# Kernel tuning notes

Measured on AMD Instinct MI355X. Metric: run time of the kernel, lower is better.

The kernel has to match this reference:

```python
import jax, jax.numpy as jnp
import numpy as np

EPS = 1e-6
PRED_LEN = 336
K_DETACH = 6

def expmap0(v):
    # tangent v [..., E] at Lorentz origin (k=1) -> point [..., E+1]
    r = jnp.linalg.norm(v, axis=-1, keepdims=True)
    x0 = jnp.cosh(r)
    scale = jnp.where(r > EPS, jnp.sinh(r) / jnp.maximum(r, EPS), 1.0)
    return jnp.concatenate([x0, scale * v], axis=-1)

def logmap0(x):
    # Lorentz point [..., E+1] -> tangent [..., E] at origin (k=1)
    x0 = jnp.clip(x[..., :1], 1.0, None)
    xs = x[..., 1:]
    r = jnp.arccosh(x0)
    n = jnp.linalg.norm(xs, axis=-1, keepdims=True)
    return r * xs / jnp.maximum(n, EPS)

def setup_inputs():
    key = jax.random.key(0)
    ks = jax.random.split(key, 16)
    B, T, C = 128, 2048, 128
    E, H, L = 32, 64, 2048
    w = lambda k, s: jax.random.normal(k, s, jnp.float32) * 0.02
    z = lambda s: jnp.zeros(s, jnp.float32)
    return dict(
        x=jax.random.normal(ks[0], (B, T, C), jnp.float32),
        We_trend=w(ks[1], (L, E)), be_trend=z((E,)),
        We_weekly=w(ks[2], (L, E)), be_weekly=z((E,)),
        We_daily=w(ks[3], (L, E)), be_daily=z((E,)),
        We_resid=w(ks[4], (L, E)), be_resid=z((E,)),
        Wd_in=w(ks[5], (E, H)), bd_in=z((H,)),
        Wd_gate=w(ks[6], (E, H)), bd_gate=z((H,)),
        Wd_out=w(ks[7], (H, E)), bd_out=z((E,)),
        Wr=w(ks[8], (E, C)), br=z((C,)),
    )

def _forward(x, We_trend, be_trend, We_weekly, be_weekly, We_daily, be_daily,
             We_resid, be_resid, Wd_in, bd_in, Wd_gate, bd_gate, Wd_out, bd_out, Wr, br):
    B, T, C = x.shape
    k = min(7, T // 4)
    if k > 1:
        xp = jnp.pad(x, ((0, 0), (k // 2, k // 2), (0, 0)), mode='edge')  # replicate pad on time
        cs = jnp.cumsum(xp, axis=1)
        cs = jnp.concatenate([jnp.zeros((B, 1, C), x.dtype), cs], axis=1)
        trend = (cs[:, k:, :] - cs[:, :-k, :]) / k  # avg_pool1d(kernel=k, stride=1) -> [B,T,C]
    else:
        trend = x
    residual = x - trend
    # only channel 0 is consumed downstream
    t0 = trend[:, :, 0]       # [B, T]
    r0 = residual[:, :, 0]    # weekly == daily == resid == residual[:, :, 0]
    # ParallelLorentzBlock: per-component lookback projection, tanh, sum, lift to Lorentz
    v = (jnp.tanh(t0 @ We_trend + be_trend)
         + jnp.tanh(r0 @ We_weekly + be_weekly)
         + jnp.tanh(r0 @ We_daily + be_daily)
         + jnp.tanh(r0 @ We_resid + be_resid))  # [B, E]
    z0 = expmap0(v)  # combined_h on Lorentz manifold [B, E+1]
    masks = ((jnp.arange(PRED_LEN) + 1) % K_DETACH) == 0

    def step(z, m):
        tv = logmap0(z)  # [B, E]
        u = jax.nn.silu(tv @ Wd_in + bd_in) * jax.nn.sigmoid(tv @ Wd_gate + bd_gate)  # gated Mamba-style update
        vn = tv + u @ Wd_out + bd_out
        zn = expmap0(vn)
        x_pred = logmap0(zn) @ Wr + br  # reconstruction head -> [B, C]
        zc = jnp.where(m, jax.lax.stop_gradient(zn), zn)  # periodic detach every K steps
        return zc, x_pred

    _, preds = jax.lax.scan(step, z0, masks)  # [pred_len, B, C]
    return jnp.transpose(preds, (1, 0, 2))    # [B, pred_len, C]

def reference(x, We_trend, be_trend, We_weekly, be_weekly, We_daily, be_daily,
              We_resid, be_resid, Wd_in, bd_in, Wd_gate, bd_gate, Wd_out, bd_out, Wr, br):
    return _forward(x, We_trend, be_trend, We_weekly, be_weekly, We_daily, be_daily,
                    We_resid, be_resid, Wd_in, bd_in, Wd_gate, bd_gate, Wd_out, bd_out, Wr, br)
```

## Files before the change

kernel.cpp:

```cpp
#include <hip/hip_runtime.h>

typedef float v2f __attribute__((ext_vector_type(2)));

#define T_LEN 2048
#define BB    128
#define CC    128
#define EE    32
#define HH    64
#define PRED  336
#define CH    28
#define NCH   12

#define WS_MAG 0
#define WS_MR  8192
#define WS_CAG 16384
#define WS_CR  16512
#define WS_V   16640

__device__ __forceinline__ v2f mk2(float a, float b) { v2f t; t.x = a; t.y = b; return t; }

__device__ __forceinline__ float swap_sum1(float X, float Y) {
    unsigned x = __builtin_bit_cast(unsigned, X);
    unsigned y = __builtin_bit_cast(unsigned, Y);
#if __has_builtin(__builtin_amdgcn_permlane32_swap)
    auto r = __builtin_amdgcn_permlane32_swap(x, y, false, false);
    return __builtin_bit_cast(float, (unsigned)r[0]) +
           __builtin_bit_cast(float, (unsigned)r[1]);
#else
    asm("v_permlane32_swap_b32 %0, %1" : "+v"(x), "+v"(y));
    return __builtin_bit_cast(float, x) + __builtin_bit_cast(float, y);
#endif
}

__device__ __forceinline__ v2f swap_sum(v2f X, v2f Y) {
    v2f z;
    z.x = swap_sum1(X.x, Y.x);
    z.y = swap_sum1(X.y, Y.y);
    return z;
}

#define ROWS(F) F(0) F(1) F(2) F(3) F(4) F(5) F(6) F(7) F(8) F(9) F(10) F(11) \
                F(12) F(13) F(14) F(15) F(16) F(17) F(18) F(19) F(20) F(21)   \
                F(22) F(23) F(24) F(25) F(26) F(27) F(28) F(29) F(30) F(31)
#define DECLM(r) v2f mA##r, mB##r;
#define INITM(r) mA##r = Mrow[(rbase + r) * HH + p];      \
                 mB##r = Mrow[(rbase + r) * HH + p + 32];
#define FMAQ(q, a, b, c, d)                               \
    X0 += q.x * mA##a;  Y0 += q.x * mB##a;                \
    X1 += q.y * mA##b;  Y1 += q.y * mB##b;                \
    X0 += q.z * mA##c;  Y0 += q.z * mB##c;                \
    X1 += q.w * mA##d;  Y1 += q.w * mB##d;
#define FMA_ALL                                           \
    FMAQ(q0,  0,  1,  2,  3)  FMAQ(q1,  4,  5,  6,  7)    \
    FMAQ(q2,  8,  9, 10, 11)  FMAQ(q3, 12, 13, 14, 15)    \
    FMAQ(q4, 16, 17, 18, 19)  FMAQ(q5, 20, 21, 22, 23)    \
    FMAQ(q6, 24, 25, 26, 27)  FMAQ(q7, 28, 29, 30, 31)

__global__ __launch_bounds__(256) void prep_kernel(
    const float* __restrict__ x,
    const float* __restrict__ WeT, const float* __restrict__ beT,
    const float* __restrict__ WeW, const float* __restrict__ beW,
    const float* __restrict__ WeD, const float* __restrict__ beD,
    const float* __restrict__ WeR, const float* __restrict__ beR,
    const float* __restrict__ Wdin, const float* __restrict__ Wdg,
    const float* __restrict__ Wdo,  const float* __restrict__ bdo,
    const float* __restrict__ Wr,
    float* __restrict__ ws)
{
    const int tid = threadIdx.x;

    if (blockIdx.x < BB) {
        __shared__ __align__(16) float s_x [T_LEN + 6];
        __shared__ __align__(16) float s_tr[T_LEN];
        __shared__ __align__(16) float s_rs[T_LEN];
        __shared__ __align__(16) float s_part[4][8][32];

        const int b = blockIdx.x;
        const float* xb = x + (size_t)b * T_LEN * CC;

        for (int i = tid; i < T_LEN + 6; i += 256) {
            int t = i - 3;
            t = t < 0 ? 0 : (t > T_LEN - 1 ? T_LEN - 1 : t);
            s_x[i] = xb[(size_t)t * CC];
        }
        __syncthreads();

        for (int t = tid; t < T_LEN; t += 256) {
            float s = 0.f;
            #pragma unroll
            for (int j = 0; j < 7; ++j) s += s_x[t + j];
            float tm = s * (1.0f / 7.0f);
            s_tr[t] = tm;
            s_rs[t] = s_x[t + 3] - tm;
        }
        __syncthreads();

        {
            const int e = tid & 31, tg = tid >> 5;
            float a0 = 0.f, a1 = 0.f, a2 = 0.f, a3 = 0.f;
            #pragma unroll 4
            for (int j = 0; j < 256; ++j) {
                int lt = tg * 256 + j;
                int wi = lt * EE + e;
                float trv = s_tr[lt], rsv = s_rs[lt];
                a0 += trv * WeT[wi];
                a1 += rsv * WeW[wi];
                a2 += rsv * WeD[wi];
                a3 += rsv * WeR[wi];
            }
            s_part[0][tg][e] = a0;
            s_part[1][tg][e] = a1;
            s_part[2][tg][e] = a2;
            s_part[3][tg][e] = a3;
        }
        __syncthreads();

        if (tid < EE) {
            float s0 = 0.f, s1 = 0.f, s2 = 0.f, s3 = 0.f;
            #pragma unroll
            for (int g = 0; g < 8; ++g) {
                s0 += s_part[0][g][tid];
                s1 += s_part[1][g][tid];
                s2 += s_part[2][g][tid];
                s3 += s_part[3][g][tid];
            }
            ws[WS_V + b * EE + tid] =
                  tanhf(s0 + beT[tid]) + tanhf(s1 + beW[tid])
                + tanhf(s2 + beD[tid]) + tanhf(s3 + beR[tid]);
        }
        return;
    }

    const int t0 = (blockIdx.x - BB) * 256 + tid;
    const int hp = t0 >> 6;
    const int j  = t0 & 63;
    float mi = 0.f, mg = 0.f, r0 = 0.f, r1 = 0.f;
    #pragma unroll 4
    for (int e = 0; e < EE; ++e) {
        float wo = Wdo[hp * EE + e];
        mi += wo * Wdin[e * HH + j];
        mg += wo * Wdg [e * HH + j];
        r0 += wo * Wr  [e * CC + 2 * j];
        r1 += wo * Wr  [e * CC + 2 * j + 1];
    }
    ws[WS_MAG + (hp * HH + j) * 2    ] = mi;
    ws[WS_MAG + (hp * HH + j) * 2 + 1] = mg;
    ws[WS_MR  + hp * CC + 2 * j      ] = r0;
    ws[WS_MR  + hp * CC + 2 * j + 1  ] = r1;

    if (t0 < HH) {
        float ci = 0.f, cg = 0.f;
        for (int e = 0; e < EE; ++e) {
            float bo = bdo[e];
            ci += bo * Wdin[e * HH + t0];
            cg += bo * Wdg [e * HH + t0];
        }
        ws[WS_CAG + t0 * 2    ] = ci;
        ws[WS_CAG + t0 * 2 + 1] = cg;
    } else if (t0 < HH + CC) {
        int c = t0 - HH;
        float cr = 0.f;
        for (int e = 0; e < EE; ++e) cr += bdo[e] * Wr[e * CC + c];
        ws[WS_CR + c] = cr;
    }
}

__global__ __launch_bounds__(128, 1) void scan_kernel(
    const float* __restrict__ ws,
    const float* __restrict__ Wdin, const float* __restrict__ bdin,
    const float* __restrict__ Wdg,  const float* __restrict__ bdg,
    const float* __restrict__ Wr,   const float* __restrict__ br,
    float* __restrict__ out)
{
    __shared__ __align__(16) float s_v[EE];
    __shared__ __align__(16) float s_u[2][CH][HH];

    const int tid  = threadIdx.x;
    const int wid  = tid >> 6;
    const int lane = tid & 63;
    const int half = lane >> 5;
    const int p    = lane & 31;
    const int b    = blockIdx.x;

    if (tid < EE) s_v[tid] = ws[WS_V + b * EE + tid];
    __syncthreads();

    if (wid == 0) {
        const v2f* Mrow = (const v2f*)(ws + WS_MAG);
        const int rbase = half << 5;
        ROWS(DECLM)
        ROWS(INITM)
        const v2f c_ag = ((const v2f*)(ws + WS_CAG))[lane];

        v2f ag = mk2(bdin[lane], bdg[lane]);
        {
            v2f t0 = mk2(0.f, 0.f), t1 = mk2(0.f, 0.f);
            for (int e = 0; e < EE; e += 2) {
                float v0 = s_v[e], v1 = s_v[e + 1];
                t0.x += v0 * Wdin[e * HH + lane];
                t0.y += v0 * Wdg [e * HH + lane];
                t1.x += v1 * Wdin[(e + 1) * HH + lane];
                t1.y += v1 * Wdg [(e + 1) * HH + lane];
            }
            ag += t0 + t1;
        }

        for (int c = 0; c < NCH + 1; ++c) {
            if (c < NCH) {
                float* ring = &s_u[c & 1][0][0];
                for (int i = 0; i < CH; ++i) {
                    float a = ag.x, g = ag.y;
                    float ea = __expf(-a), eg = __expf(-g);
                    float u = a * __builtin_amdgcn_rcpf((1.f + ea) * (1.f + eg));
                    ring[i * HH + lane] = u;

                    const float4* u4 = (const float4*)(ring + i * HH + (half << 5));
                    float4 q0 = u4[0], q1 = u4[1], q2 = u4[2], q3 = u4[3];
                    float4 q4 = u4[4], q5 = u4[5], q6 = u4[6], q7 = u4[7];
                    v2f X0 = mk2(0.f, 0.f), X1 = mk2(0.f, 0.f);
                    v2f Y0 = mk2(0.f, 0.f), Y1 = mk2(0.f, 0.f);
                    FMA_ALL
                    ag += swap_sum(X0 + X1, Y0 + Y1) + c_ag;
                }
            }
            __syncthreads();
        }
    } else {
        const v2f* Mrow = (const v2f*)(ws + WS_MR);
        const int rbase = half << 5;
        ROWS(DECLM)
        ROWS(INITM)
        const v2f c_r2 = ((const v2f*)(ws + WS_CR))[lane];

        v2f P = ((const v2f*)br)[lane];
        {
            v2f t0 = mk2(0.f, 0.f), t1 = mk2(0.f, 0.f);
            for (int e = 0; e < EE; e += 2) {
                t0 += s_v[e]     * ((const v2f*)(Wr + e * CC))[lane];
                t1 += s_v[e + 1] * ((const v2f*)(Wr + (e + 1) * CC))[lane];
            }
            P += t0 + t1;
        }

        v2f* outb = (v2f*)(out + (size_t)b * PRED * CC);

        for (int c = 0; c < NCH + 1; ++c) {
            if (c > 0) {
                const float* ring = &s_u[(c - 1) & 1][0][0];
                const int n0 = (c - 1) * CH;
                for (int i = 0; i < CH; ++i) {
                    const float4* u4 = (const float4*)(ring + i * HH + (half << 5));
                    float4 q0 = u4[0], q1 = u4[1], q2 = u4[2], q3 = u4[3];
                    float4 q4 = u4[4], q5 = u4[5], q6 = u4[6], q7 = u4[7];
                    v2f X0 = mk2(0.f, 0.f), X1 = mk2(0.f, 0.f);
                    v2f Y0 = mk2(0.f, 0.f), Y1 = mk2(0.f, 0.f);
                    FMA_ALL
                    P += swap_sum(X0 + X1, Y0 + Y1) + c_r2;
                    outb[(size_t)(n0 + i) * (CC / 2) + lane] = P;
                }
            }
            __syncthreads();
        }
    }
}

extern "C" void kernel_launch(void* const* d_in, const int* in_sizes, int n_in,
                              void* d_out, int out_size, void* d_ws, size_t ws_size,
                              hipStream_t stream)
{
    const float* x    = (const float*)d_in[0];
    const float* WeT  = (const float*)d_in[1];
    const float* beT  = (const float*)d_in[2];
    const float* WeW  = (const float*)d_in[3];
    const float* beW  = (const float*)d_in[4];
    const float* WeD  = (const float*)d_in[5];
    const float* beD  = (const float*)d_in[6];
    const float* WeR  = (const float*)d_in[7];
    const float* beR  = (const float*)d_in[8];
    const float* Wdin = (const float*)d_in[9];
    const float* bdin = (const float*)d_in[10];
    const float* Wdg  = (const float*)d_in[11];
    const float* bdg  = (const float*)d_in[12];
    const float* Wdo  = (const float*)d_in[13];
    const float* bdo  = (const float*)d_in[14];
    const float* Wr   = (const float*)d_in[15];
    const float* br   = (const float*)d_in[16];

    float* ws  = (float*)d_ws;
    float* out = (float*)d_out;

    prep_kernel<<<BB + 16, 256, 0, stream>>>(x, WeT, beT, WeW, beW, WeD, beD,
                                             WeR, beR, Wdin, Wdg, Wdo, bdo,
                                             Wr, ws);
    scan_kernel<<<BB, 128, 0, stream>>>(ws, Wdin, bdin, Wdg, bdg, Wr, br, out);
}
```

Measured before the change: 345.4 us.

## Broadcast gate activations via readlane and stream transposed weight matrix from memory

Result: slower. 353.8 us (+2.5%).

```diff
diff --git a/kernel.cpp b/kernel.cpp
--- a/kernel.cpp
+++ b/kernel.cpp
@@ -18,6 +18,14 @@
 #define WS_V   16640
 
 __device__ __forceinline__ v2f mk2(float a, float b) { v2f t; t.x = a; t.y = b; return t; }
+
+__device__ __forceinline__ float bcast(unsigned ub, int k) {
+#if __has_builtin(__builtin_amdgcn_readlane)
+    return __builtin_bit_cast(float, (unsigned)__builtin_amdgcn_readlane((int)ub, k));
+#else
+    return __builtin_bit_cast(float, (unsigned)__shfl((int)ub, k, 64));
+#endif
+}
 
 __device__ __forceinline__ float swap_sum1(float X, float Y) {
     unsigned x = __builtin_bit_cast(unsigned, X);
@@ -56,6 +64,16 @@
     FMAQ(q4, 16, 17, 18, 19)  FMAQ(q5, 20, 21, 22, 23)    \
     FMAQ(q6, 24, 25, 26, 27)  FMAQ(q7, 28, 29, 30, 31)
 
+#define PGRP(g, ACC)                                                        \
+    _Pragma("unroll")                                                       \
+    for (int k2 = 0; k2 < 8; ++k2) {                                        \
+        float4 mm = Mcol4[(g) * 8 + k2];                                    \
+        float s0 = bcast(ub, (g) * 16 + 2 * k2);                            \
+        float s1 = bcast(ub, (g) * 16 + 2 * k2 + 1);                        \
+        ACC.x += s0 * mm.x;  ACC.y += s0 * mm.y;                            \
+        ACC.x += s1 * mm.z;  ACC.y += s1 * mm.w;                            \
+    }
+
 __global__ __launch_bounds__(256) void prep_kernel(
     const float* __restrict__ x,
     const float* __restrict__ WeT, const float* __restrict__ beT,
@@ -143,8 +161,8 @@
         r0 += wo * Wr  [e * CC + 2 * j];
         r1 += wo * Wr  [e * CC + 2 * j + 1];
     }
-    ws[WS_MAG + (hp * HH + j) * 2    ] = mi;
-    ws[WS_MAG + (hp * HH + j) * 2 + 1] = mg;
+    ws[WS_MAG + (j * HH + hp) * 2    ] = mi;
+    ws[WS_MAG + (j * HH + hp) * 2 + 1] = mg;
     ws[WS_MR  + hp * CC + 2 * j      ] = r0;
     ws[WS_MR  + hp * CC + 2 * j + 1  ] = r1;
 
@@ -186,10 +204,7 @@
     __syncthreads();
 
     if (wid == 0) {
-        const v2f* Mrow = (const v2f*)(ws + WS_MAG);
-        const int rbase = half << 5;
-        ROWS(DECLM)
-        ROWS(INITM)
+        const float4* Mcol4 = (const float4*)(ws + WS_MAG) + lane * (HH / 2);
         const v2f c_ag = ((const v2f*)(ws + WS_CAG))[lane];
 
         v2f ag = mk2(bdin[lane], bdg[lane]);
@@ -214,13 +229,16 @@
                     float u = a * __builtin_amdgcn_rcpf((1.f + ea) * (1.f + eg));
                     ring[i * HH + lane] = u;
 
-                    const float4* u4 = (const float4*)(ring + i * HH + (half << 5));
-                    float4 q0 = u4[0], q1 = u4[1], q2 = u4[2], q3 = u4[3];
-                    float4 q4 = u4[4], q5 = u4[5], q6 = u4[6], q7 = u4[7];
-                    v2f X0 = mk2(0.f, 0.f), X1 = mk2(0.f, 0.f);
-                    v2f Y0 = mk2(0.f, 0.f), Y1 = mk2(0.f, 0.f);
-                    FMA_ALL
-                    ag += swap_sum(X0 + X1, Y0 + Y1) + c_ag;
+                    const unsigned ub = __builtin_bit_cast(unsigned, u);
+                    v2f A0 = c_ag;
+                    v2f A1 = mk2(0.f, 0.f);
+                    v2f A2 = mk2(0.f, 0.f);
+                    v2f A3 = mk2(0.f, 0.f);
+                    PGRP(0, A0)
+                    PGRP(1, A1)
+                    PGRP(2, A2)
+                    PGRP(3, A3)
+                    ag += (A0 + A1) + (A2 + A3);
                 }
             }
             __syncthreads();
```
